# Kernel tuning notes

Hardware: AMD Instinct MI355X
Metric: run time of the kernel (lower is better)

The kernel has to match this reference:

```python
import jax, jax.numpy as jnp
import numpy as np

T = 131072      # sequence length
I = 5           # input_size
H = 100         # hidden_layer_size
O = 1           # output_size


def setup_inputs() -> dict:
    key = jax.random.key(0)
    ks = jax.random.split(key, 7)
    s_ih = 1.0 / np.sqrt(H)
    return {
        "input_seq": jax.random.normal(ks[0], (T, I), dtype=jnp.float32),
        "W_ih": jax.random.uniform(ks[1], (4 * H, I), jnp.float32, -s_ih, s_ih),
        "W_hh": jax.random.uniform(ks[2], (4 * H, H), jnp.float32, -s_ih, s_ih),
        "b_ih": jax.random.uniform(ks[3], (4 * H,), jnp.float32, -s_ih, s_ih),
        "b_hh": jax.random.uniform(ks[4], (4 * H,), jnp.float32, -s_ih, s_ih),
        "W_lin": jax.random.uniform(ks[5], (O, H), jnp.float32, -s_ih, s_ih),
        "b_lin": jax.random.uniform(ks[6], (O,), jnp.float32, -s_ih, s_ih),
    }


def reference(input_seq, W_ih, W_hh, b_ih, b_hh, W_lin, b_lin):
    # Precompute input projections for all timesteps in one GEMM: [T, 4H]
    x_proj = input_seq @ W_ih.T + b_ih + b_hh

    def step(carry, xp_t):
        h, c = carry  # each [H]
        z = xp_t + h @ W_hh.T            # [4H], PyTorch gate order: i, f, g, o
        i = jax.nn.sigmoid(z[0 * H:1 * H])
        f = jax.nn.sigmoid(z[1 * H:2 * H])
        g = jnp.tanh(z[2 * H:3 * H])
        o = jax.nn.sigmoid(z[3 * H:4 * H])
        c = f * c + i * g
        h = o * jnp.tanh(c)
        return (h, c), None

    h0 = jnp.zeros((H,), dtype=input_seq.dtype)
    c0 = jnp.zeros((H,), dtype=input_seq.dtype)
    (h_T, _), _ = jax.lax.scan(step, (h0, c0), x_proj)
    # Original applies linear to every timestep then takes the last row;
    # mathematically identical to applying it to the final hidden state.
    return h_T @ W_lin.T + b_lin  # [O]
```

## Files before the change

### kernel.cpp

```cpp
#include <hip/hip_runtime.h>

#define T_LEN 131072
#define HDIM  100
#define KPAD  112
#define NROWS 400
#define NTHR  448
#define LOG2E 1.4426950408889634f

typedef __attribute__((ext_vector_type(2))) float f32x2;


template <int PAT>
__device__ __forceinline__ float qdpp(float v) {
    return __int_as_float(__builtin_amdgcn_mov_dpp(__float_as_int(v), PAT, 0xf, 0xf, true));
}

__global__ __launch_bounds__(256, 1)
void lstm_prep_kernel(const float* __restrict__ W_ih,
                      const float* __restrict__ W_hh,
                      const float* __restrict__ b_ih,
                      const float* __restrict__ b_hh,
                      float* __restrict__ ws)
{
    const int idx = blockIdx.x * 256 + threadIdx.x;
    if (idx >= NROWS * KPAD) return;
    const int row = idx / KPAD;
    const int col = idx - row * KPAD;
    const float sc = ((row >= 2 * HDIM) && (row < 3 * HDIM)) ? 2.f * LOG2E : LOG2E;
    float wv;
    if      (col < HDIM)      wv = W_hh[row * HDIM + col];
    else if (col < HDIM + 5)  wv = W_ih[row * 5 + (col - HDIM)];
    else if (col == HDIM + 5) wv = b_ih[row] + b_hh[row];
    else                      wv = 0.f;
    ws[idx] = wv * sc;
}

__global__ __launch_bounds__(NTHR, 1)
void lstm_seq_kernel(const float* __restrict__ input_seq,
                     const float* __restrict__ ws,
                     const float* __restrict__ W_lin,
                     const float* __restrict__ b_lin,
                     float* __restrict__ out)
{
    __shared__ __align__(16) float hbuf[2][KPAD];

    const int tid = threadIdx.x;
    const int j   = tid >> 2;
    const int g   = tid & 3;
    const bool act = j < HDIM;
    const int je  = act ? j : 0;
    const int cb  = 28 * g;

    const f32x2* __restrict__ wr0 = (const f32x2*)(ws + (0 * HDIM + je) * KPAD + cb);
    const f32x2* __restrict__ wr1 = (const f32x2*)(ws + (1 * HDIM + je) * KPAD + cb);
    const f32x2* __restrict__ wr2 = (const f32x2*)(ws + (2 * HDIM + je) * KPAD + cb);
    const f32x2* __restrict__ wr3 = (const f32x2*)(ws + (3 * HDIM + je) * KPAD + cb);
#define WLD(v, k) const f32x2 w##v##_##k = wr##v[k];
#define WROW(v) \
    WLD(v,0)  WLD(v,1)  WLD(v,2)  WLD(v,3)  WLD(v,4)  WLD(v,5)  WLD(v,6) \
    WLD(v,7)  WLD(v,8)  WLD(v,9)  WLD(v,10) WLD(v,11) WLD(v,12) WLD(v,13)
    WROW(0) WROW(1) WROW(2) WROW(3)
#undef WROW
#undef WLD

    if (tid < 2 * KPAD) ((float*)hbuf)[tid] = 0.f;
    __syncthreads();
    if (tid < 5) hbuf[0][HDIM + tid] = input_seq[tid];
    if (tid == 5) { hbuf[0][HDIM + 5] = 1.f; hbuf[1][HDIM + 5] = 1.f; }
    __syncthreads();

    float c = 0.f;

    for (int t = 0; t < T_LEN; ++t) {
        float xn = 0.f;
        if (tid < 5) {
            const int tn = (t + 1 < T_LEN) ? (t + 1) : (T_LEN - 1);
            xn = input_seq[tn * 5 + tid];
        }

        const float4* __restrict__ hp = (const float4*)(hbuf[t & 1] + cb);
        const float4 q0 = hp[0], q1 = hp[1], q2 = hp[2], q3 = hp[3];
        const float4 q4 = hp[4], q5 = hp[5], q6 = hp[6];

        f32x2 p0a = f32x2{0.f, 0.f}, p0b = f32x2{0.f, 0.f};
        f32x2 p1a = f32x2{0.f, 0.f}, p1b = f32x2{0.f, 0.f};
        f32x2 p2a = f32x2{0.f, 0.f}, p2b = f32x2{0.f, 0.f};
        f32x2 p3a = f32x2{0.f, 0.f}, p3b = f32x2{0.f, 0.f};
#define FMQ(Q, KA, KB) {                                     \
        const f32x2 hA = f32x2{Q.x, Q.y};                    \
        const f32x2 hB = f32x2{Q.z, Q.w};                    \
        p0a = hA * w0_##KA + p0a;  p0b = hB * w0_##KB + p0b; \
        p1a = hA * w1_##KA + p1a;  p1b = hB * w1_##KB + p1b; \
        p2a = hA * w2_##KA + p2a;  p2b = hB * w2_##KB + p2b; \
        p3a = hA * w3_##KA + p3a;  p3b = hB * w3_##KB + p3b; }
        FMQ(q0, 0, 1)  FMQ(q1, 2, 3)  FMQ(q2, 4, 5)  FMQ(q3, 6, 7)
        FMQ(q4, 8, 9)  FMQ(q5, 10, 11) FMQ(q6, 12, 13)
#undef FMQ
        float p0 = (p0a.x + p0a.y) + (p0b.x + p0b.y);
        float p1 = (p1a.x + p1a.y) + (p1b.x + p1b.y);
        float p2 = (p2a.x + p2a.y) + (p2b.x + p2b.y);
        float p3 = (p3a.x + p3a.y) + (p3b.x + p3b.y);

        p0 += qdpp<0xB1>(p0); p1 += qdpp<0xB1>(p1);
        p2 += qdpp<0xB1>(p2); p3 += qdpp<0xB1>(p3);
        p0 += qdpp<0x4E>(p0); p1 += qdpp<0x4E>(p1);
        p2 += qdpp<0x4E>(p2); p3 += qdpp<0x4E>(p3);

        const float si = __builtin_amdgcn_rcpf(1.f + __builtin_amdgcn_exp2f(-p0));
        const float sf = __builtin_amdgcn_rcpf(1.f + __builtin_amdgcn_exp2f(-p1));
        const float gg = fmaf(2.f, __builtin_amdgcn_rcpf(1.f + __builtin_amdgcn_exp2f(-p2)), -1.f);
        const float so = __builtin_amdgcn_rcpf(1.f + __builtin_amdgcn_exp2f(-p3));

        c = fmaf(sf, c, si * gg);
        const float th = fmaf(2.f, __builtin_amdgcn_rcpf(1.f + __builtin_amdgcn_exp2f(c * (-2.f * LOG2E))), -1.f);
        const float hv = so * th;

        float* __restrict__ hn = hbuf[(t + 1) & 1];
        if ((g == 0) & act) hn[j] = hv;
        if (tid < 5) hn[HDIM + tid] = xn;
        __syncthreads();
    }

    if (tid == 0) {
        float acc = b_lin[0];
        #pragma unroll
        for (int k = 0; k < HDIM; ++k) acc += W_lin[k] * hbuf[0][k];
        out[0] = acc;
    }
}

extern "C" void kernel_launch(void* const* d_in, const int* in_sizes, int n_in,
                              void* d_out, int out_size, void* d_ws, size_t ws_size,
                              hipStream_t stream) {
    const float* input_seq = (const float*)d_in[0];
    const float* W_ih      = (const float*)d_in[1];
    const float* W_hh      = (const float*)d_in[2];
    const float* b_ih      = (const float*)d_in[3];
    const float* b_hh      = (const float*)d_in[4];
    const float* W_lin     = (const float*)d_in[5];
    const float* b_lin     = (const float*)d_in[6];
    float* out = (float*)d_out;
    float* ws  = (float*)d_ws;

    const int nprep = NROWS * KPAD;
    lstm_prep_kernel<<<(nprep + 255) / 256, 256, 0, stream>>>(W_ih, W_hh, b_ih, b_hh, ws);
    lstm_seq_kernel<<<1, NTHR, 0, stream>>>(input_seq, ws, W_lin, b_lin, out);
}
```

Measured before the change: 71.42 ms.

## Assign two hidden units per quad to shrink block to four waves

The block drops from 448 to 256 threads, and each 4-lane group now computes two hidden units (j and j+50), keeping eight weight rows in registers instead of four. Fewer waves take part in each per-timestep barrier, which is meant to cut synchronization latency on this serial recurrence. In exchange each thread does twice the FMAs and transcendental work per step and holds twice as many weight registers, which lengthens the critical path and raises register pressure. The weights are now loaded as float4 and each gate uses a single accumulator chain, which also lengthens the dependency chain.

```diff
diff --git a/kernel.cpp b/kernel.cpp
--- a/kernel.cpp
+++ b/kernel.cpp
@@ -4,7 +4,7 @@
 #define HDIM  100
 #define KPAD  112
 #define NROWS 400
-#define NTHR  448
+#define NTHR  256
 #define LOG2E 1.4426950408889634f
 
 typedef __attribute__((ext_vector_type(2))) float f32x2;
@@ -45,23 +45,28 @@
     __shared__ __align__(16) float hbuf[2][KPAD];
 
     const int tid = threadIdx.x;
-    const int j   = tid >> 2;
+    const int q   = tid >> 2;
     const int g   = tid & 3;
-    const bool act = j < HDIM;
-    const int je  = act ? j : 0;
+    const bool act = q < 50;
+    const int jA  = act ? q : 0;
+    const int jB  = jA + 50;
     const int cb  = 28 * g;
 
-    const f32x2* __restrict__ wr0 = (const f32x2*)(ws + (0 * HDIM + je) * KPAD + cb);
-    const f32x2* __restrict__ wr1 = (const f32x2*)(ws + (1 * HDIM + je) * KPAD + cb);
-    const f32x2* __restrict__ wr2 = (const f32x2*)(ws + (2 * HDIM + je) * KPAD + cb);
-    const f32x2* __restrict__ wr3 = (const f32x2*)(ws + (3 * HDIM + je) * KPAD + cb);
-#define WLD(v, k) const f32x2 w##v##_##k = wr##v[k];
-#define WROW(v) \
-    WLD(v,0)  WLD(v,1)  WLD(v,2)  WLD(v,3)  WLD(v,4)  WLD(v,5)  WLD(v,6) \
-    WLD(v,7)  WLD(v,8)  WLD(v,9)  WLD(v,10) WLD(v,11) WLD(v,12) WLD(v,13)
-    WROW(0) WROW(1) WROW(2) WROW(3)
+    const float4* __restrict__ wp0 = (const float4*)(ws + (0 * HDIM + jA) * KPAD + cb);
+    const float4* __restrict__ wp1 = (const float4*)(ws + (1 * HDIM + jA) * KPAD + cb);
+    const float4* __restrict__ wp2 = (const float4*)(ws + (2 * HDIM + jA) * KPAD + cb);
+    const float4* __restrict__ wp3 = (const float4*)(ws + (3 * HDIM + jA) * KPAD + cb);
+    const float4* __restrict__ wp4 = (const float4*)(ws + (0 * HDIM + jB) * KPAD + cb);
+    const float4* __restrict__ wp5 = (const float4*)(ws + (1 * HDIM + jB) * KPAD + cb);
+    const float4* __restrict__ wp6 = (const float4*)(ws + (2 * HDIM + jB) * KPAD + cb);
+    const float4* __restrict__ wp7 = (const float4*)(ws + (3 * HDIM + jB) * KPAD + cb);
+#define WROW(r) \
+    const float4 w##r##_0 = wp##r[0]; const float4 w##r##_1 = wp##r[1]; \
+    const float4 w##r##_2 = wp##r[2]; const float4 w##r##_3 = wp##r[3]; \
+    const float4 w##r##_4 = wp##r[4]; const float4 w##r##_5 = wp##r[5]; \
+    const float4 w##r##_6 = wp##r[6];
+    WROW(0) WROW(1) WROW(2) WROW(3) WROW(4) WROW(5) WROW(6) WROW(7)
 #undef WROW
-#undef WLD
 
     if (tid < 2 * KPAD) ((float*)hbuf)[tid] = 0.f;
     __syncthreads();
@@ -69,7 +74,7 @@
     if (tid == 5) { hbuf[0][HDIM + 5] = 1.f; hbuf[1][HDIM + 5] = 1.f; }
     __syncthreads();
 
-    float c = 0.f;
+    float cA = 0.f, cB = 0.f;
 
     for (int t = 0; t < T_LEN; ++t) {
         float xn = 0.f;
@@ -79,46 +84,82 @@
         }
 
         const float4* __restrict__ hp = (const float4*)(hbuf[t & 1] + cb);
-        const float4 q0 = hp[0], q1 = hp[1], q2 = hp[2], q3 = hp[3];
-        const float4 q4 = hp[4], q5 = hp[5], q6 = hp[6];
 
-        f32x2 p0a = f32x2{0.f, 0.f}, p0b = f32x2{0.f, 0.f};
-        f32x2 p1a = f32x2{0.f, 0.f}, p1b = f32x2{0.f, 0.f};
-        f32x2 p2a = f32x2{0.f, 0.f}, p2b = f32x2{0.f, 0.f};
-        f32x2 p3a = f32x2{0.f, 0.f}, p3b = f32x2{0.f, 0.f};
-#define FMQ(Q, KA, KB) {                                     \
-        const f32x2 hA = f32x2{Q.x, Q.y};                    \
-        const f32x2 hB = f32x2{Q.z, Q.w};                    \
-        p0a = hA * w0_##KA + p0a;  p0b = hB * w0_##KB + p0b; \
-        p1a = hA * w1_##KA + p1a;  p1b = hB * w1_##KB + p1b; \
-        p2a = hA * w2_##KA + p2a;  p2b = hB * w2_##KB + p2b; \
-        p3a = hA * w3_##KA + p3a;  p3b = hB * w3_##KB + p3b; }
-        FMQ(q0, 0, 1)  FMQ(q1, 2, 3)  FMQ(q2, 4, 5)  FMQ(q3, 6, 7)
-        FMQ(q4, 8, 9)  FMQ(q5, 10, 11) FMQ(q6, 12, 13)
-#undef FMQ
-        float p0 = (p0a.x + p0a.y) + (p0b.x + p0b.y);
-        float p1 = (p1a.x + p1a.y) + (p1b.x + p1b.y);
-        float p2 = (p2a.x + p2a.y) + (p2b.x + p2b.y);
-        float p3 = (p3a.x + p3a.y) + (p3b.x + p3b.y);
+        f32x2 p0 = f32x2{0.f, 0.f}, p1 = f32x2{0.f, 0.f};
+        f32x2 p2 = f32x2{0.f, 0.f}, p3 = f32x2{0.f, 0.f};
+        f32x2 p4 = f32x2{0.f, 0.f}, p5 = f32x2{0.f, 0.f};
+        f32x2 p6 = f32x2{0.f, 0.f}, p7 = f32x2{0.f, 0.f};
+#define FMB(HQ, K) {                                            \
+        const f32x2 hA = f32x2{HQ.x, HQ.y};                     \
+        const f32x2 hB = f32x2{HQ.z, HQ.w};                     \
+        p0 = hA * f32x2{w0_##K.x, w0_##K.y} + p0;               \
+        p0 = hB * f32x2{w0_##K.z, w0_##K.w} + p0;               \
+        p1 = hA * f32x2{w1_##K.x, w1_##K.y} + p1;               \
+        p1 = hB * f32x2{w1_##K.z, w1_##K.w} + p1;               \
+        p2 = hA * f32x2{w2_##K.x, w2_##K.y} + p2;               \
+        p2 = hB * f32x2{w2_##K.z, w2_##K.w} + p2;               \
+        p3 = hA * f32x2{w3_##K.x, w3_##K.y} + p3;               \
+        p3 = hB * f32x2{w3_##K.z, w3_##K.w} + p3;               \
+        p4 = hA * f32x2{w4_##K.x, w4_##K.y} + p4;               \
+        p4 = hB * f32x2{w4_##K.z, w4_##K.w} + p4;               \
+        p5 = hA * f32x2{w5_##K.x, w5_##K.y} + p5;               \
+        p5 = hB * f32x2{w5_##K.z, w5_##K.w} + p5;               \
+        p6 = hA * f32x2{w6_##K.x, w6_##K.y} + p6;               \
+        p6 = hB * f32x2{w6_##K.z, w6_##K.w} + p6;               \
+        p7 = hA * f32x2{w7_##K.x, w7_##K.y} + p7;               \
+        p7 = hB * f32x2{w7_##K.z, w7_##K.w} + p7; }
+        {
+            float4 hq0 = hp[0];
+            float4 hq1 = hp[1];
+            FMB(hq0, 0)
+            float4 hq2 = hp[2];
+            FMB(hq1, 1)
+            float4 hq3 = hp[3];
+            FMB(hq2, 2)
+            float4 hq4 = hp[4];
+            FMB(hq3, 3)
+            float4 hq5 = hp[5];
+            FMB(hq4, 4)
+            float4 hq6 = hp[6];
+            FMB(hq5, 5)
+            FMB(hq6, 6)
+        }
+#undef FMB
+        float z0 = p0.x + p0.y, z1 = p1.x + p1.y;
+        float z2 = p2.x + p2.y, z3 = p3.x + p3.y;
+        float z4 = p4.x + p4.y, z5 = p5.x + p5.y;
+        float z6 = p6.x + p6.y, z7 = p7.x + p7.y;
 
-        p0 += qdpp<0xB1>(p0); p1 += qdpp<0xB1>(p1);
-        p2 += qdpp<0xB1>(p2); p3 += qdpp<0xB1>(p3);
-        p0 += qdpp<0x4E>(p0); p1 += qdpp<0x4E>(p1);
-        p2 += qdpp<0x4E>(p2); p3 += qdpp<0x4E>(p3);
+        z0 += qdpp<0xB1>(z0); z1 += qdpp<0xB1>(z1);
+        z2 += qdpp<0xB1>(z2); z3 += qdpp<0xB1>(z3);
+        z4 += qdpp<0xB1>(z4); z5 += qdpp<0xB1>(z5);
+        z6 += qdpp<0xB1>(z6); z7 += qdpp<0xB1>(z7);
+        z0 += qdpp<0x4E>(z0); z1 += qdpp<0x4E>(z1);
+        z2 += qdpp<0x4E>(z2); z3 += qdpp<0x4E>(z3);
+        z4 += qdpp<0x4E>(z4); z5 += qdpp<0x4E>(z5);
+        z6 += qdpp<0x4E>(z6); z7 += qdpp<0x4E>(z7);
 
-        const float si = __builtin_amdgcn_rcpf(1.f + __builtin_amdgcn_exp2f(-p0));
-        const float sf = __builtin_amdgcn_rcpf(1.f + __builtin_amdgcn_exp2f(-p1));
-        const float gg = fmaf(2.f, __builtin_amdgcn_rcpf(1.f + __builtin_amdgcn_exp2f(-p2)), -1.f);
-        const float so = __builtin_amdgcn_rcpf(1.f + __builtin_amdgcn_exp2f(-p3));
+        const float siA = __builtin_amdgcn_rcpf(1.f + __builtin_amdgcn_exp2f(-z0));
+        const float sfA = __builtin_amdgcn_rcpf(1.f + __builtin_amdgcn_exp2f(-z1));
+        const float ggA = fmaf(2.f, __builtin_amdgcn_rcpf(1.f + __builtin_amdgcn_exp2f(-z2)), -1.f);
+        const float soA = __builtin_amdgcn_rcpf(1.f + __builtin_amdgcn_exp2f(-z3));
+        const float siB = __builtin_amdgcn_rcpf(1.f + __builtin_amdgcn_exp2f(-z4));
+        const float sfB = __builtin_amdgcn_rcpf(1.f + __builtin_amdgcn_exp2f(-z5));
+        const float ggB = fmaf(2.f, __builtin_amdgcn_rcpf(1.f + __builtin_amdgcn_exp2f(-z6)), -1.f);
+        const float soB = __builtin_amdgcn_rcpf(1.f + __builtin_amdgcn_exp2f(-z7));
 
-        c = fmaf(sf, c, si * gg);
-        const float th = fmaf(2.f, __builtin_amdgcn_rcpf(1.f + __builtin_amdgcn_exp2f(c * (-2.f * LOG2E))), -1.f);
-        const float hv = so * th;
+        cA = fmaf(sfA, cA, siA * ggA);
+        cB = fmaf(sfB, cB, siB * ggB);
+        const float thA = fmaf(2.f, __builtin_amdgcn_rcpf(1.f + __builtin_amdgcn_exp2f(cA * (-2.f * LOG2E))), -1.f);
+        const float thB = fmaf(2.f, __builtin_amdgcn_rcpf(1.f + __builtin_amdgcn_exp2f(cB * (-2.f * LOG2E))), -1.f);
+        const float hvA = soA * thA;
+        const float hvB = soB * thB;
 
         float* __restrict__ hn = hbuf[(t + 1) & 1];
-        if ((g == 0) & act) hn[j] = hv;
+        if ((g == 0) & act) { hn[jA] = hvA; hn[jB] = hvB; }
         if (tid < 5) hn[HDIM + tid] = xn;
         __syncthreads();
+
     }
 
     if (tid == 0) {
```

New measurement: 104.9 ms. +46.9%, slower.
